# Kernel optimization log

Measured on AMD Instinct MI355X. Metric: run time of the kernel, lower is better.

## Reference

```python
import jax, jax.numpy as jnp
import numpy as np

B, S, E, H = 64, 256, 1024, 16
D = E // H  # head dim = 64


def setup_inputs() -> dict:
    key = jax.random.key(0)
    ks = jax.random.split(key, 6)
    x = jax.random.normal(ks[0], (B, S, E), dtype=jnp.float32)
    # torch nn.MultiheadAttention packed in-projection [3E, E] and biases
    sc = 1.0 / np.sqrt(E)
    in_proj_w = jax.random.normal(ks[1], (3 * E, E), dtype=jnp.float32) * sc
    in_proj_b = jax.random.normal(ks[2], (3 * E,), dtype=jnp.float32) * 0.02
    out_proj_w = jax.random.normal(ks[3], (E, E), dtype=jnp.float32) * sc
    out_proj_b = jax.random.normal(ks[4], (E,), dtype=jnp.float32) * 0.02
    # spatial bias = exp(-dist^2 / (2*median)) in (0, 1], symmetric
    pos = jax.random.normal(ks[5], (S, 3), dtype=jnp.float32)
    dist = jnp.sqrt(jnp.sum((pos[:, None, :] - pos[None, :, :]) ** 2, -1) + 1e-12)
    med = jnp.median(dist)
    spatial_bias = jnp.exp(-dist ** 2 / (2.0 * med))
    return {"x": x, "in_proj_w": in_proj_w, "in_proj_b": in_proj_b,
            "out_proj_w": out_proj_w, "out_proj_b": out_proj_b,
            "spatial_bias": spatial_bias}


def reference(x, in_proj_w, in_proj_b, out_proj_w, out_proj_b, spatial_bias):
    # packed QKV projection: x [B,S,E] @ in_proj_w.T [E,3E]
    qkv = x @ in_proj_w.T + in_proj_b          # [B,S,3E]
    q, k, v = jnp.split(qkv, 3, axis=-1)       # each [B,S,E]
    q = q.reshape(B, S, H, D)
    k = k.reshape(B, S, H, D)
    v = v.reshape(B, S, H, D)
    scale = 1.0 / jnp.sqrt(jnp.asarray(D, dtype=x.dtype))
    # additive float attn_mask broadcast over batch & heads
    scores = jnp.einsum('bqhd,bkhd->bhqk', q, k) * scale + spatial_bias[None, None]
    attn = jax.nn.softmax(scores, axis=-1)     # [B,H,S,S]
    ctx = jnp.einsum('bhqk,bkhd->bqhd', attn, v).reshape(B, S, E)
    h = ctx @ out_proj_w.T + out_proj_b        # [B,S,E]
    return x + h
```

## Files before the change

### kernel.cpp

```cpp
#include <hip/hip_runtime.h>
#include <hip/hip_bf16.h>
#include <stdint.h>


typedef __attribute__((ext_vector_type(8))) __bf16 bf16x8;
typedef __attribute__((ext_vector_type(4))) float f32x4;

#define DEVI static __device__ __forceinline__

DEVI unsigned short f2bf(float f) {
  union { float f; unsigned u; } x; x.f = f;
  unsigned r = x.u + 0x7fffu + ((x.u >> 16) & 1u);
  return (unsigned short)(r >> 16);
}

typedef unsigned int __attribute__((address_space(1))) u32_g;
typedef unsigned int __attribute__((address_space(3))) u32_l;

DEVI void g2l16(const unsigned short* g, unsigned short* l) {
  __builtin_amdgcn_global_load_lds((const u32_g*)g, (u32_l*)l, 16, 0, 0);
}

__global__ __launch_bounds__(256) void cvt_kernel(const float* __restrict__ s,
                                                  unsigned short* __restrict__ d, int n) {
  int i = (blockIdx.x * 256 + threadIdx.x) * 4;
  if (i >= n) return;
  float4 v = *(const float4*)(s + i);
  ushort4 o;
  o.x = f2bf(v.x); o.y = f2bf(v.y); o.z = f2bf(v.z); o.w = f2bf(v.w);
  *(ushort4*)(d + i) = o;
}

template <int EPI>
__global__ __launch_bounds__(256, 2)
void gemm4(const unsigned short* __restrict__ A,
           const unsigned short* __restrict__ Bw,
           const float* __restrict__ bias,
           unsigned short* __restrict__ Qo,
           unsigned short* __restrict__ Ko,
           unsigned short* __restrict__ VTo,
           const float* __restrict__ Xres,
           float* __restrict__ Out) {
  extern __shared__ unsigned short lds[];
  const int lane = threadIdx.x & 63, wid = threadIdx.x >> 6;
  const int l15 = lane & 15, lg = lane >> 4;
  const int wr = wid >> 1, wcn = wid & 1;
  const int am0 = blockIdx.x * 256, bn0 = blockIdx.y * 128;

  const int srow0 = wid * 16 + (lane >> 2);
  const int scb0  = (lane & 3) * 16;

  f32x4 acc[8][4] = {};
  bf16x8 a[8], b[4];

#define SWZ(row) ((((row) >> 1) & 3) << 4)
#define VMC(N) asm volatile("s_waitcnt vmcnt(" #N ")" ::: "memory")

#define STAGE(s) { \
    const int slot_ = (s) % 3; \
    _Pragma("unroll") \
    for (int j = 0; j < 4; ++j) { \
      const int row_ = j * 64 + srow0; \
      const int cs_ = scb0 ^ SWZ(row_); \
      g2l16(A + (size_t)(am0 + row_) * 1024 + (s) * 32 + (cs_ >> 1), \
            &lds[slot_ * 12288 + (j * 64 + wid * 16) * 32]); \
    } \
    _Pragma("unroll") \
    for (int j = 0; j < 2; ++j) { \
      const int row_ = j * 64 + srow0; \
      const int cs_ = scb0 ^ SWZ(row_); \
      g2l16(Bw + (size_t)(bn0 + row_) * 1024 + (s) * 32 + (cs_ >> 1), \
            &lds[slot_ * 12288 + 8192 + (j * 64 + wid * 16) * 32]); \
    } }

#define LOADF(p) { \
    const unsigned short* As_ = &lds[((p) % 3) * 12288]; \
    const unsigned short* Bs_ = As_ + 8192; \
    _Pragma("unroll") \
    for (int mf = 0; mf < 8; ++mf) { \
      const int row_ = wr * 128 + mf * 16 + l15; \
      a[mf] = *(const bf16x8*)((const char*)As_ + row_ * 64 + ((lg * 16) ^ SWZ(row_))); \
    } \
    _Pragma("unroll") \
    for (int nf = 0; nf < 4; ++nf) { \
      const int row_ = wcn * 64 + nf * 16 + l15; \
      b[nf] = *(const bf16x8*)((const char*)Bs_ + row_ * 64 + ((lg * 16) ^ SWZ(row_))); \
    } }

#define MM() { \
    __builtin_amdgcn_s_setprio(1); \
    _Pragma("unroll") \
    for (int mf = 0; mf < 8; ++mf) \
      _Pragma("unroll") \
      for (int nf = 0; nf < 4; ++nf) \
        acc[mf][nf] = __builtin_amdgcn_mfma_f32_16x16x32_bf16(a[mf], b[nf], acc[mf][nf], 0, 0, 0); \
    __builtin_amdgcn_s_setprio(0); }

  STAGE(0) STAGE(1)
  VMC(6);

#pragma unroll 1
  for (int p = 0; p < 32; ++p) {
    __builtin_amdgcn_s_barrier();
    if (p < 30) STAGE(p + 2)
    LOADF(p)
    asm volatile("s_waitcnt lgkmcnt(0)" ::: "memory");
    __builtin_amdgcn_sched_barrier(0);
    MM()
    if (p < 29) { VMC(6); } else { VMC(0); }
  }

  if (EPI == 0) {
#pragma unroll
    for (int nf = 0; nf < 4; ++nf) {
      const int col = bn0 + wcn * 64 + nf * 16 + l15;
      const int which = col >> 10;
      const int e = col & 1023;
      const int hh = e >> 6, dd = e & 63;
      const float bv = bias[col];
#pragma unroll
      for (int mf = 0; mf < 8; ++mf) {
        const int row0 = am0 + wr * 128 + mf * 16 + lg * 4;
        const int bb = row0 >> 8;
        const int s0 = row0 & 255;
        if (which == 2) {
          unsigned long long pk = 0;
#pragma unroll
          for (int r = 0; r < 4; ++r)
            pk |= (unsigned long long)f2bf(acc[mf][nf][r] + bv) << (16 * r);
          *(unsigned long long*)&VTo[((size_t)(bb * 16 + hh) * 64 + dd) * 256 + s0] = pk;
        } else {
          unsigned short* dst = (which == 0) ? Qo : Ko;
#pragma unroll
          for (int r = 0; r < 4; ++r)
            dst[((size_t)(bb * 16 + hh) * 256 + s0 + r) * 64 + dd] = f2bf(acc[mf][nf][r] + bv);
        }
      }
    }
  } else {
#pragma unroll
    for (int nf = 0; nf < 4; ++nf) {
      const int col = bn0 + wcn * 64 + nf * 16 + l15;
      const float bv = bias[col];
#pragma unroll
      for (int mf = 0; mf < 8; ++mf) {
#pragma unroll
        for (int r = 0; r < 4; ++r) {
          const int row = am0 + wr * 128 + mf * 16 + lg * 4 + r;
          const size_t idx = (size_t)row * 1024 + col;
          Out[idx] = Xres[idx] + acc[mf][nf][r] + bv;
        }
      }
    }
  }
#undef SWZ
#undef VMC
#undef STAGE
#undef LOADF
#undef MM
}

__global__ __launch_bounds__(256, 2)
void attn_kernel(const unsigned short* __restrict__ Qg,
                 const unsigned short* __restrict__ Kg,
                 const unsigned short* __restrict__ VTg,
                 const float* __restrict__ bias,
                 unsigned short* __restrict__ ctx) {
  __shared__ unsigned short P[4][64][40];
  const int lane = threadIdx.x & 63, wave = threadIdx.x >> 6;
  const int l15 = lane & 15, lg = lane >> 4;
  const int bh = blockIdx.x;
  const int bb = bh >> 4, hh = bh & 15;
  const size_t base = (size_t)bh * (256 * 64);
  const int q0 = wave * 64;

  bf16x8 qfr[4][2];
#pragma unroll
  for (int qi = 0; qi < 4; ++qi)
#pragma unroll
    for (int kc = 0; kc < 2; ++kc)
      qfr[qi][kc] = *(const bf16x8*)&Qg[base + (size_t)(q0 + qi * 16 + l15) * 64 + kc * 32 + lg * 8];

  f32x4 o[4][4] = {};
  float mrow[4], lrow[4];
#pragma unroll
  for (int i = 0; i < 4; ++i) { mrow[i] = -1e30f; lrow[i] = 0.f; }

  bf16x8 kfA[2][2], kfB[2][2];
#pragma unroll
  for (int kr = 0; kr < 2; ++kr)
#pragma unroll
    for (int kc = 0; kc < 2; ++kc)
      kfA[kr][kc] = *(const bf16x8*)&Kg[base + (size_t)(kr * 16 + l15) * 64 + kc * 32 + lg * 8];

#define CHUNK(c, KC, KN, PRE) { \
    const int ck = (c) * 32; \
    f32x4 b4[2][4]; \
    _Pragma("unroll") \
    for (int kr = 0; kr < 2; ++kr) \
      _Pragma("unroll") \
      for (int qi = 0; qi < 4; ++qi) \
        b4[kr][qi] = *(const f32x4*)&bias[(q0 + qi * 16 + l15) * 256 + ck + kr * 16 + lg * 4]; \
    f32x4 s[2][4] = {}; \
    _Pragma("unroll") \
    for (int kr = 0; kr < 2; ++kr) \
      _Pragma("unroll") \
      for (int qi = 0; qi < 4; ++qi) \
        _Pragma("unroll") \
        for (int kc = 0; kc < 2; ++kc) \
          s[kr][qi] = __builtin_amdgcn_mfma_f32_16x16x32_bf16(KC[kr][kc], qfr[qi][kc], s[kr][qi], 0, 0, 0); \
    if (PRE) { \
      _Pragma("unroll") \
      for (int kr = 0; kr < 2; ++kr) \
        _Pragma("unroll") \
        for (int kc = 0; kc < 2; ++kc) \
          KN[kr][kc] = *(const bf16x8*)&Kg[base + (size_t)(ck + 32 + kr * 16 + l15) * 64 + kc * 32 + lg * 8]; \
    } \
    bf16x8 vb[4]; \
    _Pragma("unroll") \
    for (int df = 0; df < 4; ++df) \
      vb[df] = *(const bf16x8*)&VTg[base + (size_t)(df * 16 + l15) * 256 + ck + lg * 8]; \
    float cmax[4]; \
    _Pragma("unroll") \
    for (int qi = 0; qi < 4; ++qi) cmax[qi] = -1e30f; \
    _Pragma("unroll") \
    for (int kr = 0; kr < 2; ++kr) \
      _Pragma("unroll") \
      for (int qi = 0; qi < 4; ++qi) \
        _Pragma("unroll") \
        for (int r = 0; r < 4; ++r) { \
          float v = s[kr][qi][r] * 0.125f + b4[kr][qi][r]; \
          s[kr][qi][r] = v; \
          cmax[qi] = fmaxf(cmax[qi], v); \
        } \
    _Pragma("unroll") \
    for (int qi = 0; qi < 4; ++qi) { \
      cmax[qi] = fmaxf(cmax[qi], __shfl_xor(cmax[qi], 16, 64)); \
      cmax[qi] = fmaxf(cmax[qi], __shfl_xor(cmax[qi], 32, 64)); \
    } \
    float resc[4], csum[4]; \
    _Pragma("unroll") \
    for (int qi = 0; qi < 4; ++qi) { \
      float mn = fmaxf(mrow[qi], cmax[qi]); \
      resc[qi] = __expf(mrow[qi] - mn); \
      mrow[qi] = mn; \
      csum[qi] = 0.f; \
    } \
    _Pragma("unroll") \
    for (int kr = 0; kr < 2; ++kr) \
      _Pragma("unroll") \
      for (int qi = 0; qi < 4; ++qi) \
        _Pragma("unroll") \
        for (int r = 0; r < 4; ++r) { \
          float e = __expf(s[kr][qi][r] - mrow[qi]); \
          s[kr][qi][r] = e; \
          csum[qi] += e; \
        } \
    _Pragma("unroll") \
    for (int qi = 0; qi < 4; ++qi) { \
      csum[qi] += __shfl_xor(csum[qi], 16, 64); \
      csum[qi] += __shfl_xor(csum[qi], 32, 64); \
      lrow[qi] = lrow[qi] * resc[qi] + csum[qi]; \
    } \
    _Pragma("unroll") \
    for (int kr = 0; kr < 2; ++kr) \
      _Pragma("unroll") \
      for (int qi = 0; qi < 4; ++qi) { \
        unsigned long long pk = 0; \
        _Pragma("unroll") \
        for (int r = 0; r < 4; ++r) \
          pk |= (unsigned long long)f2bf(s[kr][qi][r]) << (16 * r); \
        *(unsigned long long*)&P[wave][qi * 16 + l15][kr * 16 + lg * 4] = pk; \
      } \
    asm volatile("s_waitcnt lgkmcnt(0)" ::: "memory"); \
    _Pragma("unroll") \
    for (int qrf = 0; qrf < 4; ++qrf) \
      _Pragma("unroll") \
      for (int r = 0; r < 4; ++r) { \
        float f = __shfl(resc[qrf], lg * 4 + r, 64); \
        _Pragma("unroll") \
        for (int df = 0; df < 4; ++df) o[qrf][df][r] *= f; \
      } \
    bf16x8 pa[4]; \
    _Pragma("unroll") \
    for (int qrf = 0; qrf < 4; ++qrf) \
      pa[qrf] = *(const bf16x8*)&P[wave][qrf * 16 + l15][lg * 8]; \
    _Pragma("unroll") \
    for (int qrf = 0; qrf < 4; ++qrf) \
      _Pragma("unroll") \
      for (int df = 0; df < 4; ++df) \
        o[qrf][df] = __builtin_amdgcn_mfma_f32_16x16x32_bf16(pa[qrf], vb[df], o[qrf][df], 0, 0, 0); \
  }

#pragma unroll 1
  for (int c2 = 0; c2 < 4; ++c2) {
    CHUNK(2 * c2,     kfA, kfB, 1)
    CHUNK(2 * c2 + 1, kfB, kfA, (c2 < 3))
  }
#undef CHUNK

#pragma unroll
  for (int qrf = 0; qrf < 4; ++qrf)
#pragma unroll
    for (int r = 0; r < 4; ++r) {
      float li = __shfl(lrow[qrf], lg * 4 + r, 64);
      float inv = 1.0f / li;
      const int q = q0 + qrf * 16 + lg * 4 + r;
#pragma unroll
      for (int df = 0; df < 4; ++df) {
        const int d = df * 16 + l15;
        ctx[((size_t)(bb * 256 + q) * 16 + hh) * 64 + d] = f2bf(o[qrf][df][r] * inv);
      }
    }
}

extern "C" void kernel_launch(void* const* d_in, const int* in_sizes, int n_in,
                              void* d_out, int out_size, void* d_ws, size_t ws_size,
                              hipStream_t stream) {
  const float* x  = (const float*)d_in[0];
  const float* wi = (const float*)d_in[1];
  const float* bi = (const float*)d_in[2];
  const float* wo = (const float*)d_in[3];
  const float* bo = (const float*)d_in[4];
  const float* sb = (const float*)d_in[5];
  float* out = (float*)d_out;

  char* ws = (char*)d_ws;
  unsigned short* xbf  = (unsigned short*)(ws);
  unsigned short* winb = (unsigned short*)(ws + 33554432u);
  unsigned short* wob  = (unsigned short*)(ws + 39845888u);
  unsigned short* Qb   = (unsigned short*)(ws + 41943040u);
  unsigned short* Kb   = (unsigned short*)(ws + 75497472u);
  unsigned short* VTb  = (unsigned short*)(ws + 109051904u);
  unsigned short* ctx  = xbf;

  (void)hipFuncSetAttribute(reinterpret_cast<const void*>(gemm4<0>),
                            hipFuncAttributeMaxDynamicSharedMemorySize, 73728);
  (void)hipFuncSetAttribute(reinterpret_cast<const void*>(gemm4<1>),
                            hipFuncAttributeMaxDynamicSharedMemorySize, 73728);

  cvt_kernel<<<16384, 256, 0, stream>>>(x, xbf, 16777216);
  cvt_kernel<<<3072, 256, 0, stream>>>(wi, winb, 3145728);
  cvt_kernel<<<1024, 256, 0, stream>>>(wo, wob, 1048576);

  gemm4<0><<<dim3(64, 24), 256, 73728, stream>>>(xbf, winb, bi, Qb, Kb, VTb, nullptr, nullptr);

  attn_kernel<<<1024, 256, 0, stream>>>(Qb, Kb, VTb, sb, ctx);

  gemm4<1><<<dim3(64, 8), 256, 73728, stream>>>(ctx, wob, bo, nullptr, nullptr, nullptr, x, out);
}
```

Before: 310.8 us.

## Fuse x conversion into QKV GEMM, stage K in LDS, lazy softmax rescale

Replaces the triple-buffered 256x128 GEMM with a simpler 128x128 tile GEMM that can convert fp32 x to bf16 while loading, removing the separate x conversion pass. Folds the 1/sqrt(D) scale into Q. Stores the spatial bias as bf16 in reused workspace. In attention, stages all of K in LDS and prefetches V instead of K. Adds deferred max rescaling that skips rescaling unless the running max grows by more than 8. These cut memory traffic and ALU work, but the GEMM loses its deep software pipeline, the bf16 bias adds rounding, and the bias buffer overwrites winb after QKV uses it.

New measurement: 317.6 us. 2.2% more time.

```diff
diff --git a/kernel.cpp b/kernel.cpp
--- a/kernel.cpp
+++ b/kernel.cpp
@@ -12,6 +12,10 @@
   union { float f; unsigned u; } x; x.f = f;
   unsigned r = x.u + 0x7fffu + ((x.u >> 16) & 1u);
   return (unsigned short)(r >> 16);
+}
+
+DEVI float bf2f(unsigned short h) {
+  union { unsigned u; float f; } x; x.u = (unsigned)h << 16; return x.f;
 }
 
 typedef unsigned int __attribute__((address_space(1))) u32_g;
@@ -31,96 +35,88 @@
   *(ushort4*)(d + i) = o;
 }
 
-template <int EPI>
+template <int EPI, int AF32>
 __global__ __launch_bounds__(256, 2)
-void gemm4(const unsigned short* __restrict__ A,
-           const unsigned short* __restrict__ Bw,
-           const float* __restrict__ bias,
-           unsigned short* __restrict__ Qo,
-           unsigned short* __restrict__ Ko,
-           unsigned short* __restrict__ VTo,
-           const float* __restrict__ Xres,
-           float* __restrict__ Out) {
-  extern __shared__ unsigned short lds[];
-  const int lane = threadIdx.x & 63, wid = threadIdx.x >> 6;
+void gemm_bt(const unsigned short* __restrict__ Abf,
+             const float* __restrict__ Af,
+             const unsigned short* __restrict__ Bw,
+             const float* __restrict__ bias,
+             unsigned short* __restrict__ Qo,
+             unsigned short* __restrict__ Ko,
+             unsigned short* __restrict__ VTo,
+             const float* __restrict__ Xres,
+             float* __restrict__ Out) {
+  __shared__ unsigned short As[8192];
+  __shared__ unsigned short Bs[8192];
+  const int lane = threadIdx.x & 63, wave = threadIdx.x >> 6;
   const int l15 = lane & 15, lg = lane >> 4;
-  const int wr = wid >> 1, wcn = wid & 1;
-  const int am0 = blockIdx.x * 256, bn0 = blockIdx.y * 128;
-
-  const int srow0 = wid * 16 + (lane >> 2);
-  const int scb0  = (lane & 3) * 16;
-
-  f32x4 acc[8][4] = {};
-  bf16x8 a[8], b[4];
-
-#define SWZ(row) ((((row) >> 1) & 3) << 4)
-#define VMC(N) asm volatile("s_waitcnt vmcnt(" #N ")" ::: "memory")
-
-#define STAGE(s) { \
-    const int slot_ = (s) % 3; \
-    _Pragma("unroll") \
-    for (int j = 0; j < 4; ++j) { \
-      const int row_ = j * 64 + srow0; \
-      const int cs_ = scb0 ^ SWZ(row_); \
-      g2l16(A + (size_t)(am0 + row_) * 1024 + (s) * 32 + (cs_ >> 1), \
-            &lds[slot_ * 12288 + (j * 64 + wid * 16) * 32]); \
-    } \
-    _Pragma("unroll") \
-    for (int j = 0; j < 2; ++j) { \
-      const int row_ = j * 64 + srow0; \
-      const int cs_ = scb0 ^ SWZ(row_); \
-      g2l16(Bw + (size_t)(bn0 + row_) * 1024 + (s) * 32 + (cs_ >> 1), \
-            &lds[slot_ * 12288 + 8192 + (j * 64 + wid * 16) * 32]); \
-    } }
-
-#define LOADF(p) { \
-    const unsigned short* As_ = &lds[((p) % 3) * 12288]; \
-    const unsigned short* Bs_ = As_ + 8192; \
-    _Pragma("unroll") \
-    for (int mf = 0; mf < 8; ++mf) { \
-      const int row_ = wr * 128 + mf * 16 + l15; \
-      a[mf] = *(const bf16x8*)((const char*)As_ + row_ * 64 + ((lg * 16) ^ SWZ(row_))); \
-    } \
-    _Pragma("unroll") \
-    for (int nf = 0; nf < 4; ++nf) { \
-      const int row_ = wcn * 64 + nf * 16 + l15; \
-      b[nf] = *(const bf16x8*)((const char*)Bs_ + row_ * 64 + ((lg * 16) ^ SWZ(row_))); \
-    } }
-
-#define MM() { \
-    __builtin_amdgcn_s_setprio(1); \
-    _Pragma("unroll") \
-    for (int mf = 0; mf < 8; ++mf) \
-      _Pragma("unroll") \
-      for (int nf = 0; nf < 4; ++nf) \
-        acc[mf][nf] = __builtin_amdgcn_mfma_f32_16x16x32_bf16(a[mf], b[nf], acc[mf][nf], 0, 0, 0); \
-    __builtin_amdgcn_s_setprio(0); }
-
-  STAGE(0) STAGE(1)
-  VMC(6);
-
-#pragma unroll 1
-  for (int p = 0; p < 32; ++p) {
-    __builtin_amdgcn_s_barrier();
-    if (p < 30) STAGE(p + 2)
-    LOADF(p)
-    asm volatile("s_waitcnt lgkmcnt(0)" ::: "memory");
-    __builtin_amdgcn_sched_barrier(0);
-    MM()
-    if (p < 29) { VMC(6); } else { VMC(0); }
+  const int wr = wave >> 1, wc = wave & 1;
+  const int am0 = blockIdx.x * 128, bn0 = blockIdx.y * 128;
+
+  const int srow8 = lane >> 3;
+  const int sgsrc = (lane & 7) ^ srow8;
+
+  f32x4 acc[4][4] = {};
+
+  for (int kt = 0; kt < 16; ++kt) {
+    const int k0 = kt * 64;
+#pragma unroll
+    for (int i = 0; i < 4; ++i) {
+      const int seg = wave * 4 + i;
+      const int row = seg * 8 + srow8;
+      if (AF32) {
+        const float* p = Af + (size_t)(am0 + row) * 1024 + k0 + (lane & 7) * 8;
+        float4 v0 = *(const float4*)p;
+        float4 v1 = *(const float4*)(p + 4);
+        unsigned long long lo = (unsigned long long)f2bf(v0.x)
+          | ((unsigned long long)f2bf(v0.y) << 16)
+          | ((unsigned long long)f2bf(v0.z) << 32)
+          | ((unsigned long long)f2bf(v0.w) << 48);
+        unsigned long long hi = (unsigned long long)f2bf(v1.x)
+          | ((unsigned long long)f2bf(v1.y) << 16)
+          | ((unsigned long long)f2bf(v1.z) << 32)
+          | ((unsigned long long)f2bf(v1.w) << 48);
+        unsigned long long* d = (unsigned long long*)&As[row * 64 + (((lane & 7) ^ srow8) << 3)];
+        d[0] = lo; d[1] = hi;
+      } else {
+        g2l16(Abf + (size_t)(am0 + row) * 1024 + k0 + sgsrc * 8, &As[seg * 512]);
+      }
+      g2l16(Bw + (size_t)(bn0 + row) * 1024 + k0 + sgsrc * 8, &Bs[seg * 512]);
+    }
+    __syncthreads();
+#pragma unroll
+    for (int kk = 0; kk < 2; ++kk) {
+      bf16x8 a[4], b[4];
+#pragma unroll
+      for (int mf = 0; mf < 4; ++mf) {
+        const int row_ = wr * 64 + mf * 16 + l15;
+        a[mf] = *(const bf16x8*)((const char*)As + row_ * 128 + (((kk * 4 + lg) ^ (row_ & 7)) << 4));
+      }
+#pragma unroll
+      for (int nf = 0; nf < 4; ++nf) {
+        const int row_ = wc * 64 + nf * 16 + l15;
+        b[nf] = *(const bf16x8*)((const char*)Bs + row_ * 128 + (((kk * 4 + lg) ^ (row_ & 7)) << 4));
+      }
+#pragma unroll
+      for (int mf = 0; mf < 4; ++mf)
+#pragma unroll
+        for (int nf = 0; nf < 4; ++nf)
+          acc[mf][nf] = __builtin_amdgcn_mfma_f32_16x16x32_bf16(a[mf], b[nf], acc[mf][nf], 0, 0, 0);
+    }
+    __syncthreads();
   }
 
   if (EPI == 0) {
 #pragma unroll
     for (int nf = 0; nf < 4; ++nf) {
-      const int col = bn0 + wcn * 64 + nf * 16 + l15;
+      const int col = bn0 + wc * 64 + nf * 16 + l15;
       const int which = col >> 10;
       const int e = col & 1023;
       const int hh = e >> 6, dd = e & 63;
       const float bv = bias[col];
 #pragma unroll
-      for (int mf = 0; mf < 8; ++mf) {
-        const int row0 = am0 + wr * 128 + mf * 16 + lg * 4;
+      for (int mf = 0; mf < 4; ++mf) {
+        const int row0 = am0 + wr * 64 + mf * 16 + lg * 4;
         const int bb = row0 >> 8;
         const int s0 = row0 & 255;
         if (which == 2) {
@@ -129,43 +125,42 @@
           for (int r = 0; r < 4; ++r)
             pk |= (unsigned long long)f2bf(acc[mf][nf][r] + bv) << (16 * r);
           *(unsigned long long*)&VTo[((size_t)(bb * 16 + hh) * 64 + dd) * 256 + s0] = pk;
+        } else if (which == 0) {
+#pragma unroll
+          for (int r = 0; r < 4; ++r)
+            Qo[((size_t)(bb * 16 + hh) * 256 + s0 + r) * 64 + dd] = f2bf((acc[mf][nf][r] + bv) * 0.125f);
         } else {
-          unsigned short* dst = (which == 0) ? Qo : Ko;
 #pragma unroll
           for (int r = 0; r < 4; ++r)
-            dst[((size_t)(bb * 16 + hh) * 256 + s0 + r) * 64 + dd] = f2bf(acc[mf][nf][r] + bv);
+            Ko[((size_t)(bb * 16 + hh) * 256 + s0 + r) * 64 + dd] = f2bf(acc[mf][nf][r] + bv);
         }
       }
     }
   } else {
 #pragma unroll
     for (int nf = 0; nf < 4; ++nf) {
-      const int col = bn0 + wcn * 64 + nf * 16 + l15;
+      const int col = bn0 + wc * 64 + nf * 16 + l15;
       const float bv = bias[col];
 #pragma unroll
-      for (int mf = 0; mf < 8; ++mf) {
+      for (int mf = 0; mf < 4; ++mf) {
 #pragma unroll
         for (int r = 0; r < 4; ++r) {
-          const int row = am0 + wr * 128 + mf * 16 + lg * 4 + r;
+          const int row = am0 + wr * 64 + mf * 16 + lg * 4 + r;
           const size_t idx = (size_t)row * 1024 + col;
           Out[idx] = Xres[idx] + acc[mf][nf][r] + bv;
         }
       }
     }
   }
-#undef SWZ
-#undef VMC
-#undef STAGE
-#undef LOADF
-#undef MM
 }
 
 __global__ __launch_bounds__(256, 2)
 void attn_kernel(const unsigned short* __restrict__ Qg,
                  const unsigned short* __restrict__ Kg,
                  const unsigned short* __restrict__ VTg,
-                 const float* __restrict__ bias,
+                 const unsigned short* __restrict__ biasbf,
                  unsigned short* __restrict__ ctx) {
+  __shared__ unsigned short Ks[256 * 64];
   __shared__ unsigned short P[4][64][40];
   const int lane = threadIdx.x & 63, wave = threadIdx.x >> 6;
   const int l15 = lane & 15, lg = lane >> 4;
@@ -174,6 +169,17 @@
   const size_t base = (size_t)bh * (256 * 64);
   const int q0 = wave * 64;
 
+#pragma unroll
+  for (int j = 0; j < 8; ++j) {
+    const int r0 = (wave * 8 + j) * 8;
+    const int row = r0 + (lane >> 3);
+    const int gsrc = (lane & 7) ^ (row & 7);
+    g2l16(&Kg[base + (size_t)row * 64 + gsrc * 8], &Ks[r0 * 64]);
+  }
+  asm volatile("s_waitcnt vmcnt(0)" ::: "memory");
+  __builtin_amdgcn_sched_barrier(0);
+  __builtin_amdgcn_s_barrier();
+
   bf16x8 qfr[4][2];
 #pragma unroll
   for (int qi = 0; qi < 4; ++qi)
@@ -186,66 +192,79 @@
 #pragma unroll
   for (int i = 0; i < 4; ++i) { mrow[i] = -1e30f; lrow[i] = 0.f; }
 
-  bf16x8 kfA[2][2], kfB[2][2];
-#pragma unroll
-  for (int kr = 0; kr < 2; ++kr)
-#pragma unroll
-    for (int kc = 0; kc < 2; ++kc)
-      kfA[kr][kc] = *(const bf16x8*)&Kg[base + (size_t)(kr * 16 + l15) * 64 + kc * 32 + lg * 8];
-
-#define CHUNK(c, KC, KN, PRE) { \
+  bf16x8 vbA[4], vbB[4];
+#pragma unroll
+  for (int df = 0; df < 4; ++df)
+    vbA[df] = *(const bf16x8*)&VTg[base + (size_t)(df * 16 + l15) * 256 + lg * 8];
+
+#define CHUNKA(c, VC, VN, PRE) { \
     const int ck = (c) * 32; \
-    f32x4 b4[2][4]; \
+    if (PRE) { \
+      _Pragma("unroll") \
+      for (int df = 0; df < 4; ++df) \
+        VN[df] = *(const bf16x8*)&VTg[base + (size_t)(df * 16 + l15) * 256 + ck + 32 + lg * 8]; \
+    } \
+    ushort4 bbf[2][4]; \
     _Pragma("unroll") \
     for (int kr = 0; kr < 2; ++kr) \
       _Pragma("unroll") \
       for (int qi = 0; qi < 4; ++qi) \
-        b4[kr][qi] = *(const f32x4*)&bias[(q0 + qi * 16 + l15) * 256 + ck + kr * 16 + lg * 4]; \
+        bbf[kr][qi] = *(const ushort4*)&biasbf[(q0 + qi * 16 + l15) * 256 + ck + kr * 16 + lg * 4]; \
+    bf16x8 kf[2][2]; \
+    _Pragma("unroll") \
+    for (int kr = 0; kr < 2; ++kr) \
+      _Pragma("unroll") \
+      for (int kc = 0; kc < 2; ++kc) { \
+        const int row = ck + kr * 16 + l15; \
+        const int g = (kc * 4 + lg) ^ (row & 7); \
+        kf[kr][kc] = *(const bf16x8*)&Ks[row * 64 + g * 8]; \
+      } \
     f32x4 s[2][4] = {}; \
+    __builtin_amdgcn_s_setprio(1); \
     _Pragma("unroll") \
     for (int kr = 0; kr < 2; ++kr) \
       _Pragma("unroll") \
       for (int qi = 0; qi < 4; ++qi) \
         _Pragma("unroll") \
         for (int kc = 0; kc < 2; ++kc) \
-          s[kr][qi] = __builtin_amdgcn_mfma_f32_16x16x32_bf16(KC[kr][kc], qfr[qi][kc], s[kr][qi], 0, 0, 0); \
-    if (PRE) { \
-      _Pragma("unroll") \
-      for (int kr = 0; kr < 2; ++kr) \
-        _Pragma("unroll") \
-        for (int kc = 0; kc < 2; ++kc) \
-          KN[kr][kc] = *(const bf16x8*)&Kg[base + (size_t)(ck + 32 + kr * 16 + l15) * 64 + kc * 32 + lg * 8]; \
-    } \
-    bf16x8 vb[4]; \
-    _Pragma("unroll") \
-    for (int df = 0; df < 4; ++df) \
-      vb[df] = *(const bf16x8*)&VTg[base + (size_t)(df * 16 + l15) * 256 + ck + lg * 8]; \
+          s[kr][qi] = __builtin_amdgcn_mfma_f32_16x16x32_bf16(kf[kr][kc], qfr[qi][kc], s[kr][qi], 0, 0, 0); \
+    __builtin_amdgcn_s_setprio(0); \
     float cmax[4]; \
     _Pragma("unroll") \
     for (int qi = 0; qi < 4; ++qi) cmax[qi] = -1e30f; \
     _Pragma("unroll") \
     for (int kr = 0; kr < 2; ++kr) \
       _Pragma("unroll") \
-      for (int qi = 0; qi < 4; ++qi) \
+      for (int qi = 0; qi < 4; ++qi) { \
+        const unsigned short* bp = (const unsigned short*)&bbf[kr][qi]; \
         _Pragma("unroll") \
         for (int r = 0; r < 4; ++r) { \
-          float v = s[kr][qi][r] * 0.125f + b4[kr][qi][r]; \
+          float v = s[kr][qi][r] + bf2f(bp[r]); \
           s[kr][qi][r] = v; \
           cmax[qi] = fmaxf(cmax[qi], v); \
         } \
+      } \
     _Pragma("unroll") \
     for (int qi = 0; qi < 4; ++qi) { \
       cmax[qi] = fmaxf(cmax[qi], __shfl_xor(cmax[qi], 16, 64)); \
       cmax[qi] = fmaxf(cmax[qi], __shfl_xor(cmax[qi], 32, 64)); \
     } \
-    float resc[4], csum[4]; \
+    int defer = 1; \
+    _Pragma("unroll") \
+    for (int qi = 0; qi < 4; ++qi) defer &= (cmax[qi] - mrow[qi] <= 8.f); \
+    const int full = !__all(defer); \
+    float resc[4]; \
     _Pragma("unroll") \
     for (int qi = 0; qi < 4; ++qi) { \
-      float mn = fmaxf(mrow[qi], cmax[qi]); \
-      resc[qi] = __expf(mrow[qi] - mn); \
-      mrow[qi] = mn; \
-      csum[qi] = 0.f; \
-    } \
+      if (full) { \
+        float mn = fmaxf(mrow[qi], cmax[qi]); \
+        resc[qi] = __expf(mrow[qi] - mn); \
+        mrow[qi] = mn; \
+      } else resc[qi] = 1.f; \
+    } \
+    float csum[4]; \
+    _Pragma("unroll") \
+    for (int qi = 0; qi < 4; ++qi) csum[qi] = 0.f; \
     _Pragma("unroll") \
     for (int kr = 0; kr < 2; ++kr) \
       _Pragma("unroll") \
@@ -273,31 +292,35 @@
         *(unsigned long long*)&P[wave][qi * 16 + l15][kr * 16 + lg * 4] = pk; \
       } \
     asm volatile("s_waitcnt lgkmcnt(0)" ::: "memory"); \
-    _Pragma("unroll") \
-    for (int qrf = 0; qrf < 4; ++qrf) \
-      _Pragma("unroll") \
-      for (int r = 0; r < 4; ++r) { \
-        float f = __shfl(resc[qrf], lg * 4 + r, 64); \
-        _Pragma("unroll") \
-        for (int df = 0; df < 4; ++df) o[qrf][df][r] *= f; \
-      } \
+    if (full) { \
+      _Pragma("unroll") \
+      for (int qrf = 0; qrf < 4; ++qrf) \
+        _Pragma("unroll") \
+        for (int r = 0; r < 4; ++r) { \
+          float f = __shfl(resc[qrf], lg * 4 + r, 64); \
+          _Pragma("unroll") \
+          for (int df = 0; df < 4; ++df) o[qrf][df][r] *= f; \
+        } \
+    } \
     bf16x8 pa[4]; \
     _Pragma("unroll") \
     for (int qrf = 0; qrf < 4; ++qrf) \
       pa[qrf] = *(const bf16x8*)&P[wave][qrf * 16 + l15][lg * 8]; \
+    __builtin_amdgcn_s_setprio(1); \
     _Pragma("unroll") \
     for (int qrf = 0; qrf < 4; ++qrf) \
       _Pragma("unroll") \
       for (int df = 0; df < 4; ++df) \
-        o[qrf][df] = __builtin_amdgcn_mfma_f32_16x16x32_bf16(pa[qrf], vb[df], o[qrf][df], 0, 0, 0); \
+        o[qrf][df] = __builtin_amdgcn_mfma_f32_16x16x32_bf16(pa[qrf], VC[df], o[qrf][df], 0, 0, 0); \
+    __builtin_amdgcn_s_setprio(0); \
   }
 
 #pragma unroll 1
   for (int c2 = 0; c2 < 4; ++c2) {
-    CHUNK(2 * c2,     kfA, kfB, 1)
-    CHUNK(2 * c2 + 1, kfB, kfA, (c2 < 3))
-  }
-#undef CHUNK
+    CHUNKA(2 * c2,     vbA, vbB, 1)
+    CHUNKA(2 * c2 + 1, vbB, vbA, (c2 < 3))
+  }
+#undef CHUNKA
 
 #pragma unroll
   for (int qrf = 0; qrf < 4; ++qrf)
@@ -326,26 +349,22 @@
   float* out = (float*)d_out;
 
   char* ws = (char*)d_ws;
-  unsigned short* xbf  = (unsigned short*)(ws);
+  unsigned short* ctx  = (unsigned short*)(ws);
   unsigned short* winb = (unsigned short*)(ws + 33554432u);
   unsigned short* wob  = (unsigned short*)(ws + 39845888u);
   unsigned short* Qb   = (unsigned short*)(ws + 41943040u);
   unsigned short* Kb   = (unsigned short*)(ws + 75497472u);
   unsigned short* VTb  = (unsigned short*)(ws + 109051904u);
-  unsigned short* ctx  = xbf;
-
-  (void)hipFuncSetAttribute(reinterpret_cast<const void*>(gemm4<0>),
-                            hipFuncAttributeMaxDynamicSharedMemorySize, 73728);
-  (void)hipFuncSetAttribute(reinterpret_cast<const void*>(gemm4<1>),
-                            hipFuncAttributeMaxDynamicSharedMemorySize, 73728);
-
-  cvt_kernel<<<16384, 256, 0, stream>>>(x, xbf, 16777216);
+  unsigned short* sbbf = winb;
+
   cvt_kernel<<<3072, 256, 0, stream>>>(wi, winb, 3145728);
   cvt_kernel<<<1024, 256, 0, stream>>>(wo, wob, 1048576);
 
-  gemm4<0><<<dim3(64, 24), 256, 73728, stream>>>(xbf, winb, bi, Qb, Kb, VTb, nullptr, nullptr);
-
-  attn_kernel<<<1024, 256, 0, stream>>>(Qb, Kb, VTb, sb, ctx);
-
-  gemm4<1><<<dim3(64, 8), 256, 73728, stream>>>(ctx, wob, bo, nullptr, nullptr, nullptr, x, out);
-}
+  gemm_bt<0, 1><<<dim3(128, 24), 256, 0, stream>>>(nullptr, x, winb, bi, Qb, Kb, VTb, nullptr, nullptr);
+
+  cvt_kernel<<<64, 256, 0, stream>>>(sb, sbbf, 65536);
+
+  attn_kernel<<<1024, 256, 0, stream>>>(Qb, Kb, VTb, sbbf, ctx);
+
+  gemm_bt<1, 0><<<dim3(128, 8), 256, 0, stream>>>(ctx, nullptr, wob, bo, nullptr, nullptr, nullptr, x, out);
+}
```
